# Kernel optimization log

Hardware: AMD Instinct MI355X
Metric: run time of the kernel (lower is better)

## Reference

```python
import jax, jax.numpy as jnp
import numpy as np

B, S, HID = 2, 1024, 2048
HQ, HKV, HD = 32, 8, 64
ROPE_BASE = 10000.0

def _rope_tables(seq_len, head_dim):
    inv_freq = 1.0 / (ROPE_BASE ** (np.arange(0, head_dim, 2, dtype=np.float32) / head_dim))
    t = np.arange(seq_len, dtype=np.float32)
    freqs = np.outer(t, inv_freq)                      # [S, d/2]
    emb = np.concatenate([freqs, freqs], axis=-1)      # [S, d]
    return jnp.asarray(np.cos(emb)), jnp.asarray(np.sin(emb))

def setup_inputs() -> dict:
    key = jax.random.key(0)
    ks = jax.random.split(key, 5)
    cos, sin = _rope_tables(S, HD)
    return {
        'hidden_states': jax.random.normal(ks[0], (B, S, HID), jnp.float32),
        'cos': cos, 'sin': sin,
        'Wq': jax.random.normal(ks[1], (HID, HID), jnp.float32) * (HID ** -0.5),
        'Wk': jax.random.normal(ks[2], (HID, HKV * HD), jnp.float32) * (HID ** -0.5),
        'Wv': jax.random.normal(ks[3], (HID, HKV * HD), jnp.float32) * (HID ** -0.5),
        'Wo': jax.random.normal(ks[4], (HID, HID), jnp.float32) * (HID ** -0.5),
    }

def _rotate_half(x):
    d = x.shape[-1]
    return jnp.concatenate([-x[..., d // 2:], x[..., :d // 2]], axis=-1)

def reference(hidden_states, cos, sin, Wq, Wk, Wv, Wo):
    b, s, _ = hidden_states.shape
    q = (hidden_states @ Wq).reshape(b, s, HQ, HD)    # [b,s,Hq,d]
    k = (hidden_states @ Wk).reshape(b, s, HKV, HD)   # [b,s,Hkv,d]
    v = (hidden_states @ Wv).reshape(b, s, HKV, HD)
    # RoPE: cos/sin [s,d] broadcast as [s,1,d] over head dim
    c = cos[:, None, :]
    sn = sin[:, None, :]
    q = q * c + _rotate_half(q) * sn
    k = k * c + _rotate_half(k) * sn
    # GQA: expand kv heads to query heads (repeat_kv)
    n_rep = HQ // HKV
    k = jnp.repeat(k, n_rep, axis=2)                  # [b,s,Hq,d]
    v = jnp.repeat(v, n_rep, axis=2)
    scale = HD ** -0.5
    scores = jnp.einsum('bqhd,bkhd->bhqk', q, k) * scale  # [b,Hq,s,s]
    causal = jnp.tril(jnp.ones((s, s), bool))
    scores = jnp.where(causal, scores, jnp.float32(-1e30))
    probs = jax.nn.softmax(scores.astype(jnp.float32), axis=-1).astype(q.dtype)
    out = jnp.einsum('bhqk,bkhd->bqhd', probs, v).reshape(b, s, HID)
    return out @ Wo
```

## Files before the change

kernel.cpp:

```cpp
#include <hip/hip_runtime.h>
#include <math.h>

#define B_   2
#define S_   1024
#define HID_ 2048
#define HQ_  32
#define HKV_ 8
#define HD_  64
#define NQKV 3072

using short8  = __attribute__((ext_vector_type(8))) short;
using floatx4 = __attribute__((ext_vector_type(4))) float;

__device__ __forceinline__ unsigned short f2bf(float x) {
    unsigned int u = __builtin_bit_cast(unsigned int, x);
    u += 0x7FFFu + ((u >> 16) & 1u);
    return (unsigned short)(u >> 16);
}
__device__ __forceinline__ float bf2f(unsigned short u) {
    return __builtin_bit_cast(float, (unsigned int)u << 16);
}

__device__ __forceinline__ void gl_lds16(const unsigned short* g, unsigned short* l) {
    __builtin_amdgcn_global_load_lds(
        (const __attribute__((address_space(1))) void*)g,
        (__attribute__((address_space(3))) void*)l, 16, 0, 0);
}

__global__ __launch_bounds__(256) void gemm_qkv(const unsigned short* __restrict__ A,
                                                const unsigned short* __restrict__ Bt,
                                                unsigned short* __restrict__ Qp,
                                                unsigned short* __restrict__ KVp) {
    __shared__ __align__(16) unsigned short As[128 * 32];
    __shared__ __align__(16) unsigned short Bs[128 * 32];

    int bid = blockIdx.x;
    int m0, n0, z, Nw, nc0;
    unsigned short* C;
    if (bid < 512) {
        n0 = (bid & 15) * 128; m0 = ((bid >> 4) & 15) * 128; z = bid >> 8;
        C = Qp + (size_t)z * 2048 * 2048; Nw = 2048; nc0 = n0;
    } else {
        bid -= 512;
        n0 = 2048 + (bid & 7) * 128; m0 = ((bid >> 3) & 15) * 128; z = bid >> 7;
        C = KVp + (size_t)z * 2048 * 1024; Nw = 1024; nc0 = n0 - 2048;
    }
    const int kbase = z * 1024;

    const int tid  = threadIdx.x;
    const int w    = tid >> 6;
    const int lane = tid & 63;
    const int col  = lane & 15;
    const int quad = lane >> 4;
    const int wm = (w >> 1) * 64;
    const int wn = (w & 1) * 64;

    const int srow = lane >> 2;
    const int skof = (lane & 3) * 8;
    const unsigned short* Ag = A  + (size_t)(m0 + srow) * HID_ + skof;
    const unsigned short* Bg = Bt + (size_t)(n0 + srow) * HID_ + skof;
    const int rb = w * 16;

    floatx4 acc[4][4] = {};

    for (int k0 = kbase; k0 < kbase + 1024; k0 += 32) {
        gl_lds16(Ag + (size_t)(rb     ) * HID_ + k0, &As[(rb     ) * 32]);
        gl_lds16(Ag + (size_t)(rb + 64) * HID_ + k0, &As[(rb + 64) * 32]);
        gl_lds16(Bg + (size_t)(rb     ) * HID_ + k0, &Bs[(rb     ) * 32]);
        gl_lds16(Bg + (size_t)(rb + 64) * HID_ + k0, &Bs[(rb + 64) * 32]);
        __syncthreads();

        short8 af[4], bfr[4];
#pragma unroll
        for (int i = 0; i < 4; ++i)
            af[i] = *(const short8*)&As[(wm + i * 16 + col) * 32 + quad * 8];
#pragma unroll
        for (int j = 0; j < 4; ++j)
            bfr[j] = *(const short8*)&Bs[(wn + j * 16 + col) * 32 + quad * 8];
#pragma unroll
        for (int i = 0; i < 4; ++i)
#pragma unroll
            for (int j = 0; j < 4; ++j)
                acc[i][j] = __builtin_amdgcn_mfma_f32_16x16x32_bf16(
                    af[i], bfr[j], acc[i][j], 0, 0, 0);
        __syncthreads();
    }

#pragma unroll
    for (int i = 0; i < 4; ++i)
#pragma unroll
        for (int j = 0; j < 4; ++j)
#pragma unroll
            for (int r = 0; r < 4; ++r)
                C[(size_t)(m0 + wm + i * 16 + quad * 4 + r) * Nw
                  + (nc0 + wn + j * 16 + col)] = f2bf(acc[i][j][r]);
}

__global__ __launch_bounds__(256) void gemm_wo(const unsigned short* __restrict__ A,
                                               const unsigned short* __restrict__ Bt,
                                               float* __restrict__ Cf,
                                               unsigned short* __restrict__ Cp1) {
    __shared__ __align__(16) unsigned short As[128 * 32];
    __shared__ __align__(16) unsigned short Bs[128 * 32];

    const int m0 = blockIdx.y * 128;
    const int n0 = blockIdx.x * 128;
    const int z  = blockIdx.z;
    const int kbase = z * 1024;

    const int tid  = threadIdx.x;
    const int w    = tid >> 6;
    const int lane = tid & 63;
    const int col  = lane & 15;
    const int quad = lane >> 4;
    const int wm = (w >> 1) * 64;
    const int wn = (w & 1) * 64;

    const int srow = lane >> 2;
    const int skof = (lane & 3) * 8;
    const unsigned short* Ag = A  + (size_t)(m0 + srow) * HID_ + skof;
    const unsigned short* Bg = Bt + (size_t)(n0 + srow) * HID_ + skof;
    const int rb = w * 16;

    floatx4 acc[4][4] = {};

    for (int k0 = kbase; k0 < kbase + 1024; k0 += 32) {
        gl_lds16(Ag + (size_t)(rb     ) * HID_ + k0, &As[(rb     ) * 32]);
        gl_lds16(Ag + (size_t)(rb + 64) * HID_ + k0, &As[(rb + 64) * 32]);
        gl_lds16(Bg + (size_t)(rb     ) * HID_ + k0, &Bs[(rb     ) * 32]);
        gl_lds16(Bg + (size_t)(rb + 64) * HID_ + k0, &Bs[(rb + 64) * 32]);
        __syncthreads();

        short8 af[4], bfr[4];
#pragma unroll
        for (int i = 0; i < 4; ++i)
            af[i] = *(const short8*)&As[(wm + i * 16 + col) * 32 + quad * 8];
#pragma unroll
        for (int j = 0; j < 4; ++j)
            bfr[j] = *(const short8*)&Bs[(wn + j * 16 + col) * 32 + quad * 8];
#pragma unroll
        for (int i = 0; i < 4; ++i)
#pragma unroll
            for (int j = 0; j < 4; ++j)
                acc[i][j] = __builtin_amdgcn_mfma_f32_16x16x32_bf16(
                    af[i], bfr[j], acc[i][j], 0, 0, 0);
        __syncthreads();
    }

#pragma unroll
    for (int i = 0; i < 4; ++i)
#pragma unroll
        for (int j = 0; j < 4; ++j)
#pragma unroll
            for (int r = 0; r < 4; ++r) {
                size_t off = (size_t)(m0 + wm + i * 16 + quad * 4 + r) * HID_
                           + (n0 + wn + j * 16 + col);
                if (z == 0) Cf[off] = acc[i][j][r];
                else        Cp1[off] = f2bf(acc[i][j][r]);
            }
}

__global__ __launch_bounds__(256) void reduce_wo(float* __restrict__ out,
                                                 const unsigned short* __restrict__ p1) {
    int i4 = (blockIdx.x * 256 + threadIdx.x) * 4;
    float4 o = *(float4*)&out[i4];
    ushort4 p = *(const ushort4*)&p1[i4];
    o.x += bf2f(p.x); o.y += bf2f(p.y); o.z += bf2f(p.z); o.w += bf2f(p.w);
    *(float4*)&out[i4] = o;
}

__global__ __launch_bounds__(256) void convert_x(const float* __restrict__ in,
                                                 unsigned short* __restrict__ out) {
    int tid = blockIdx.x * 256 + threadIdx.x;
    float4 v = *(const float4*)&in[(size_t)tid * 4];
    ushort4 o = {f2bf(v.x), f2bf(v.y), f2bf(v.z), f2bf(v.w)};
    *(ushort4*)&out[(size_t)tid * 4] = o;
}

__global__ __launch_bounds__(256) void transpose_qkv(const float* __restrict__ Wq,
                                                     const float* __restrict__ Wk,
                                                     const float* __restrict__ Wv,
                                                     unsigned short* __restrict__ WcatT) {
    __shared__ float tile[32][33];
    int bid = blockIdx.x;
    const float* W;
    unsigned short* WT;
    int N, tn0, tk0;
    if (bid < 4096) {
        W = Wq; WT = WcatT; N = HID_;
        tn0 = (bid & 63) * 32; tk0 = (bid >> 6) * 32;
    } else if (bid < 5120) {
        bid -= 4096;
        W = Wk; WT = WcatT + (size_t)HID_ * HID_; N = 512;
        tn0 = (bid & 15) * 32; tk0 = (bid >> 4) * 32;
    } else {
        bid -= 5120;
        W = Wv; WT = WcatT + (size_t)(HID_ + 512) * HID_; N = 512;
        tn0 = (bid & 15) * 32; tk0 = (bid >> 4) * 32;
    }
    const int r  = threadIdx.x >> 3;
    const int c4 = (threadIdx.x & 7) * 4;
    float4 v = *(const float4*)&W[(size_t)(tk0 + r) * N + tn0 + c4];
    tile[r][c4 + 0] = v.x;
    tile[r][c4 + 1] = v.y;
    tile[r][c4 + 2] = v.z;
    tile[r][c4 + 3] = v.w;
    __syncthreads();
    ushort4 o = {f2bf(tile[c4 + 0][r]), f2bf(tile[c4 + 1][r]),
                 f2bf(tile[c4 + 2][r]), f2bf(tile[c4 + 3][r])};
    *(ushort4*)&WT[(size_t)(tn0 + r) * HID_ + tk0 + c4] = o;
}

__global__ __launch_bounds__(256) void transpose_wo(const float* __restrict__ Wo,
                                                    unsigned short* __restrict__ WoT) {
    __shared__ float tile[32][33];
    int bid = blockIdx.x;
    const int tn0 = (bid & 63) * 32;
    const int tk0 = (bid >> 6) * 32;
    const int r  = threadIdx.x >> 3;
    const int c4 = (threadIdx.x & 7) * 4;
    float4 v = *(const float4*)&Wo[(size_t)(tk0 + r) * HID_ + tn0 + c4];
    tile[r][c4 + 0] = v.x;
    tile[r][c4 + 1] = v.y;
    tile[r][c4 + 2] = v.z;
    tile[r][c4 + 3] = v.w;
    __syncthreads();
    ushort4 o = {f2bf(tile[c4 + 0][r]), f2bf(tile[c4 + 1][r]),
                 f2bf(tile[c4 + 2][r]), f2bf(tile[c4 + 3][r])};
    *(ushort4*)&WoT[(size_t)(tn0 + r) * HID_ + tk0 + c4] = o;
}

__global__ __launch_bounds__(256) void convert_qkv(const unsigned short* __restrict__ Qp,
                                                   const unsigned short* __restrict__ KVp,
                                                   const float* __restrict__ cosT,
                                                   const float* __restrict__ sinT,
                                                   unsigned short* __restrict__ Qbf,
                                                   unsigned short* __restrict__ Kbf,
                                                   unsigned short* __restrict__ Vt) {
    const size_t QSTR  = (size_t)2048 * 2048;
    const size_t KVSTR = (size_t)2048 * 1024;
    int tid = blockIdx.x * 256 + threadIdx.x;
    const int NQ = B_ * S_ * HQ_ * 32;
    const int NK = B_ * S_ * HKV_ * 32;
    if (tid < NQ) {
        int d = tid & 31;
        int h = (tid >> 5) & (HQ_ - 1);
        int s = (tid >> 10) & (S_ - 1);
        int b = tid >> 20;
        const unsigned short* row = Qp + (size_t)(b * S_ + s) * 2048 + h * HD_;
        float x0 = bf2f(row[d])      + bf2f(row[QSTR + d]);
        float x1 = bf2f(row[d + 32]) + bf2f(row[QSTR + d + 32]);
        float c0 = cosT[s * HD_ + d],      s0 = sinT[s * HD_ + d];
        float c1 = cosT[s * HD_ + d + 32], s1 = sinT[s * HD_ + d + 32];
        unsigned short* orow = Qbf + ((size_t)(b * HQ_ + h) * S_ + s) * HD_;
        orow[d]      = f2bf((x0 * c0 - x1 * s0) * 0.125f);
        orow[d + 32] = f2bf((x1 * c1 + x0 * s1) * 0.125f);
    } else if (tid < NQ + NK) {
        tid -= NQ;
        int d  = tid & 31;
        int kv = (tid >> 5) & (HKV_ - 1);
        int s  = (tid >> 8) & (S_ - 1);
        int b  = tid >> 18;
        const unsigned short* row = KVp + (size_t)(b * S_ + s) * 1024 + kv * HD_;
        float x0 = bf2f(row[d])      + bf2f(row[KVSTR + d]);
        float x1 = bf2f(row[d + 32]) + bf2f(row[KVSTR + d + 32]);
        float c0 = cosT[s * HD_ + d],      s0 = sinT[s * HD_ + d];
        float c1 = cosT[s * HD_ + d + 32], s1 = sinT[s * HD_ + d + 32];
        unsigned short* orow = Kbf + ((size_t)(b * HKV_ + kv) * S_ + s) * HD_;
        orow[d]      = f2bf(x0 * c0 - x1 * s0);
        orow[d + 32] = f2bf(x1 * c1 + x0 * s1);
    } else {
        tid -= NQ + NK;
        int s4 = tid & 255;
        int d  = (tid >> 8) & (HD_ - 1);
        int kv = (tid >> 14) & (HKV_ - 1);
        int b  = tid >> 17;
        int s  = s4 * 4;
        const unsigned short* base =
            KVp + ((size_t)(b * S_ + s)) * 1024 + 512 + kv * HD_ + d;
        ushort4 o;
#pragma unroll
        for (int j = 0; j < 4; ++j) {
            float v = bf2f(base[(size_t)j * 1024]) +
                      bf2f(base[KVSTR + (size_t)j * 1024]);
            ((unsigned short*)&o)[j] = f2bf(v);
        }
        *(ushort4*)&Vt[((size_t)(b * HKV_ + kv) * HD_ + d) * S_ + s] = o;
    }
}

__global__ __launch_bounds__(256) void attn_mfma(const unsigned short* __restrict__ Qbf,
                                                 const unsigned short* __restrict__ Kbf,
                                                 const unsigned short* __restrict__ Vt,
                                                 unsigned short* __restrict__ Ctx) {
    const int t  = 63 - blockIdx.x;
    const int kv = blockIdx.y;
    const int b  = blockIdx.z;
    const int w    = threadIdx.x >> 6;
    const int lane = threadIdx.x & 63;
    const int col  = lane & 15;
    const int quad = lane >> 4;

    const int h   = kv * 4 + w;
    const int bh  = b * HQ_ + h;
    const int bkv = b * HKV_ + kv;
    const int qw  = 16 * t;
    const int myq = qw + col;

    __shared__ __align__(16) unsigned short sK[2][64 * 32];
    __shared__ __align__(16) unsigned short sV[2][64 * 32];
    __shared__ __align__(16) unsigned short sP[4][16 * 72];
    unsigned short* myP = sP[w];

    const unsigned short* qrow = Qbf + ((size_t)bh * S_ + qw + col) * HD_;
    short8 bq0 = *(const short8*)&qrow[quad * 8];
    short8 bq1 = *(const short8*)&qrow[32 + quad * 8];

    const unsigned short* Kbase = Kbf + (size_t)bkv * S_ * HD_;
    const unsigned short* Vbase = Vt  + (size_t)bkv * HD_ * S_;

    const int srow = 16 * w + (lane >> 2);
    const int sch  = (lane & 3) * 8;
    unsigned short* dK0 = &sK[0][16 * w * 32];
    unsigned short* dK1 = &sK[1][16 * w * 32];
    unsigned short* dV0 = &sV[0][16 * w * 32];
    unsigned short* dV1 = &sV[1][16 * w * 32];

    floatx4 acc[4] = {};
    float m_i = -1e30f, l_i = 0.f;
    const int nsteps = (16 * t + 79) >> 6;

    for (int it = 0; it < nsteps; ++it) {
        const int k0 = it * 64;
        gl_lds16(Kbase + (size_t)(k0 + srow) * HD_ + sch,      dK0);
        gl_lds16(Kbase + (size_t)(k0 + srow) * HD_ + 32 + sch, dK1);
        gl_lds16(Vbase + (size_t)srow * S_ + k0 + sch,         dV0);
        gl_lds16(Vbase + (size_t)srow * S_ + k0 + 32 + sch,    dV1);
        __syncthreads();

        floatx4 sc[4];
#pragma unroll
        for (int tt = 0; tt < 4; ++tt) {
            short8 ak0 = *(const short8*)&sK[0][(16 * tt + col) * 32 + quad * 8];
            short8 ak1 = *(const short8*)&sK[1][(16 * tt + col) * 32 + quad * 8];
            floatx4 z = {0.f, 0.f, 0.f, 0.f};
            z = __builtin_amdgcn_mfma_f32_16x16x32_bf16(ak0, bq0, z, 0, 0, 0);
            z = __builtin_amdgcn_mfma_f32_16x16x32_bf16(ak1, bq1, z, 0, 0, 0);
            sc[tt] = z;
        }
        if (k0 + 63 > qw) {
#pragma unroll
            for (int tt = 0; tt < 4; ++tt)
#pragma unroll
                for (int r = 0; r < 4; ++r)
                    if (k0 + 16 * tt + quad * 4 + r > myq) sc[tt][r] = -1e30f;
        }
        float vmax = sc[0][0];
#pragma unroll
        for (int tt = 0; tt < 4; ++tt)
#pragma unroll
            for (int r = 0; r < 4; ++r)
                vmax = fmaxf(vmax, sc[tt][r]);
        vmax = fmaxf(vmax, __shfl_xor(vmax, 16, 64));
        vmax = fmaxf(vmax, __shfl_xor(vmax, 32, 64));
        const float mnew  = fmaxf(m_i, vmax);
        const float alpha = __expf(m_i - mnew);
        m_i = mnew;
        float lsum = 0.f;
#pragma unroll
        for (int tt = 0; tt < 4; ++tt) {
            float p0 = __expf(sc[tt][0] - mnew);
            float p1 = __expf(sc[tt][1] - mnew);
            float p2 = __expf(sc[tt][2] - mnew);
            float p3 = __expf(sc[tt][3] - mnew);
            lsum += (p0 + p1) + (p2 + p3);
            ushort4 pk = {f2bf(p0), f2bf(p1), f2bf(p2), f2bf(p3)};
            *(ushort4*)&myP[col * 72 + 16 * tt + quad * 4] = pk;
        }
        lsum += __shfl_xor(lsum, 16, 64);
        lsum += __shfl_xor(lsum, 32, 64);
        l_i = l_i * alpha + lsum;
        float a_r[4];
#pragma unroll
        for (int r = 0; r < 4; ++r)
            a_r[r] = __shfl(alpha, quad * 4 + r, 64);
#pragma unroll
        for (int nt = 0; nt < 4; ++nt)
#pragma unroll
            for (int r = 0; r < 4; ++r)
                acc[nt][r] *= a_r[r];
        short8 pa0 = *(const short8*)&myP[col * 72 + quad * 8];
        short8 pa1 = *(const short8*)&myP[col * 72 + 32 + quad * 8];
#pragma unroll
        for (int nt = 0; nt < 4; ++nt) {
            short8 vb0 = *(const short8*)&sV[0][(nt * 16 + col) * 32 + quad * 8];
            short8 vb1 = *(const short8*)&sV[1][(nt * 16 + col) * 32 + quad * 8];
            acc[nt] = __builtin_amdgcn_mfma_f32_16x16x32_bf16(pa0, vb0, acc[nt], 0, 0, 0);
            acc[nt] = __builtin_amdgcn_mfma_f32_16x16x32_bf16(pa1, vb1, acc[nt], 0, 0, 0);
        }
        __syncthreads();
    }

    const float invl = 1.0f / l_i;
    float inv_r[4];
#pragma unroll
    for (int r = 0; r < 4; ++r)
        inv_r[r] = __shfl(invl, quad * 4 + r, 64);
#pragma unroll
    for (int nt = 0; nt < 4; ++nt)
#pragma unroll
        for (int r = 0; r < 4; ++r)
            Ctx[(size_t)(b * S_ + qw + quad * 4 + r) * HID_ + h * HD_ + nt * 16 + col] =
                f2bf(acc[nt][r] * inv_r[r]);
}

extern "C" void kernel_launch(void* const* d_in, const int* in_sizes, int n_in,
                              void* d_out, int out_size, void* d_ws, size_t ws_size,
                              hipStream_t stream) {
    const float* X    = (const float*)d_in[0];
    const float* cosT = (const float*)d_in[1];
    const float* sinT = (const float*)d_in[2];
    const float* Wq   = (const float*)d_in[3];
    const float* Wk   = (const float*)d_in[4];
    const float* Wv   = (const float*)d_in[5];
    const float* Wo   = (const float*)d_in[6];

    const int M = B_ * S_;
    const size_t MB = 1024u * 1024u;

    char* ws = (char*)d_ws;
    unsigned short* Xbf   = (unsigned short*)(ws);
    unsigned short* Qbf   = (unsigned short*)(ws);
    unsigned short* WcatT = (unsigned short*)(ws + 8 * MB);
    unsigned short* Kbf   = (unsigned short*)(ws + 8 * MB);
    unsigned short* Vt    = (unsigned short*)(ws + 10 * MB);
    unsigned short* WoT   = (unsigned short*)(ws + 12 * MB);
    unsigned short* KVp   = (unsigned short*)(ws + 20 * MB);
    unsigned short* Ctxbf = (unsigned short*)(ws + 20 * MB);
    unsigned short* Wop1  = (unsigned short*)(ws);
    unsigned short* Qp    = (unsigned short*)d_out;
    float* out = (float*)d_out;

    convert_x<<<(M * HID_ / 4) / 256, 256, 0, stream>>>(X, Xbf);

    transpose_qkv<<<6144, 256, 0, stream>>>(Wq, Wk, Wv, WcatT);

    gemm_qkv<<<768, 256, 0, stream>>>(Xbf, WcatT, Qp, KVp);

    {
        int total = B_ * S_ * HQ_ * 32 + B_ * S_ * HKV_ * 32
                  + B_ * HKV_ * HD_ * (S_ / 4);
        convert_qkv<<<total / 256, 256, 0, stream>>>(Qp, KVp, cosT, sinT,
                                                     Qbf, Kbf, Vt);
    }

    transpose_wo<<<4096, 256, 0, stream>>>(Wo, WoT);

    attn_mfma<<<dim3(64, HKV_, B_), 256, 0, stream>>>(Qbf, Kbf, Vt, Ctxbf);

    gemm_wo<<<dim3(16, 16, 2), 256, 0, stream>>>(Ctxbf, WoT, out, Wop1);

    reduce_wo<<<(M * HID_ / 4) / 256, 256, 0, stream>>>(out, Wop1);
}
```

Baseline: 246.9 us.

## Double-buffer K/V tiles, process two query tiles per wave, swizzle LDS

The attention kernel now gives each wave 32 query rows instead of 16, reusing every K/V LDS tile across two MFMA query tiles and halving the grid. K/V tiles are double-buffered, so the next tile's global-to-LDS load is issued before computing on the current one. LDS rows are widened to 64 elements with an XOR swizzle to avoid bank conflicts, and s_setprio raises priority around the MFMA sections. Costs are more registers and LDS per block and fewer blocks, which may lower occupancy and worsen load balance under the causal mask.

```diff
diff --git a/kernel.cpp b/kernel.cpp
--- a/kernel.cpp
+++ b/kernel.cpp
@@ -293,7 +293,7 @@
                                                  const unsigned short* __restrict__ Kbf,
                                                  const unsigned short* __restrict__ Vt,
                                                  unsigned short* __restrict__ Ctx) {
-    const int t  = 63 - blockIdx.x;
+    const int tq = 31 - blockIdx.x;
     const int kv = blockIdx.y;
     const int b  = blockIdx.z;
     const int w    = threadIdx.x >> 6;
@@ -304,114 +304,162 @@
     const int h   = kv * 4 + w;
     const int bh  = b * HQ_ + h;
     const int bkv = b * HKV_ + kv;
-    const int qw  = 16 * t;
-    const int myq = qw + col;
-
-    __shared__ __align__(16) unsigned short sK[2][64 * 32];
-    __shared__ __align__(16) unsigned short sV[2][64 * 32];
-    __shared__ __align__(16) unsigned short sP[4][16 * 72];
+    const int qw  = 32 * tq;
+
+    __shared__ __align__(16) unsigned short sK[2][64 * 64];
+    __shared__ __align__(16) unsigned short sV[2][64 * 64];
+    __shared__ __align__(16) unsigned short sP[4][32 * 72];
     unsigned short* myP = sP[w];
 
-    const unsigned short* qrow = Qbf + ((size_t)bh * S_ + qw + col) * HD_;
-    short8 bq0 = *(const short8*)&qrow[quad * 8];
-    short8 bq1 = *(const short8*)&qrow[32 + quad * 8];
+    short8 bq[2][2];
+#pragma unroll
+    for (int u = 0; u < 2; ++u) {
+        const unsigned short* qrow = Qbf + ((size_t)bh * S_ + qw + 16 * u + col) * HD_;
+        bq[u][0] = *(const short8*)&qrow[quad * 8];
+        bq[u][1] = *(const short8*)&qrow[32 + quad * 8];
+    }
 
     const unsigned short* Kbase = Kbf + (size_t)bkv * S_ * HD_;
     const unsigned short* Vbase = Vt  + (size_t)bkv * HD_ * S_;
 
-    const int srow = 16 * w + (lane >> 2);
-    const int sch  = (lane & 3) * 8;
-    unsigned short* dK0 = &sK[0][16 * w * 32];
-    unsigned short* dK1 = &sK[1][16 * w * 32];
-    unsigned short* dV0 = &sV[0][16 * w * 32];
-    unsigned short* dV1 = &sV[1][16 * w * 32];
-
-    floatx4 acc[4] = {};
-    float m_i = -1e30f, l_i = 0.f;
-    const int nsteps = (16 * t + 79) >> 6;
-
+    const int sr  = lane >> 3;
+    const int ssl = (lane & 7) ^ sr;
+    const int r0  = 16 * w;
+
+    floatx4 acc[2][4] = {};
+    float m_i[2] = {-1e30f, -1e30f};
+    float l_i[2] = {0.f, 0.f};
+
+    const int nsteps = (qw + 95) >> 6;
+
+#pragma unroll
+    for (int c = 0; c < 2; ++c) {
+        const int row = r0 + 8 * c + sr;
+        gl_lds16(Kbase + (size_t)row * HD_ + ssl * 8, &sK[0][(r0 + 8 * c) * 64]);
+        gl_lds16(Vbase + (size_t)row * S_ + ssl * 8,  &sV[0][(r0 + 8 * c) * 64]);
+    }
+    __syncthreads();
+
+    int cur = 0;
     for (int it = 0; it < nsteps; ++it) {
         const int k0 = it * 64;
-        gl_lds16(Kbase + (size_t)(k0 + srow) * HD_ + sch,      dK0);
-        gl_lds16(Kbase + (size_t)(k0 + srow) * HD_ + 32 + sch, dK1);
-        gl_lds16(Vbase + (size_t)srow * S_ + k0 + sch,         dV0);
-        gl_lds16(Vbase + (size_t)srow * S_ + k0 + 32 + sch,    dV1);
+
+        if (it + 1 < nsteps) {
+            const int kn = k0 + 64;
+#pragma unroll
+            for (int c = 0; c < 2; ++c) {
+                const int row = r0 + 8 * c + sr;
+                gl_lds16(Kbase + (size_t)(kn + row) * HD_ + ssl * 8,
+                         &sK[cur ^ 1][(r0 + 8 * c) * 64]);
+                gl_lds16(Vbase + (size_t)row * S_ + kn + ssl * 8,
+                         &sV[cur ^ 1][(r0 + 8 * c) * 64]);
+            }
+        }
+
+        floatx4 sc[2][4];
+        __builtin_amdgcn_s_setprio(1);
+#pragma unroll
+        for (int tt = 0; tt < 4; ++tt) {
+            const int krow = 16 * tt + col;
+            const unsigned short* kr = &sK[cur][krow * 64];
+            short8 ak0 = *(const short8*)&kr[((quad    ) ^ (krow & 7)) * 8];
+            short8 ak1 = *(const short8*)&kr[((quad + 4) ^ (krow & 7)) * 8];
+#pragma unroll
+            for (int u = 0; u < 2; ++u) {
+                floatx4 z = {0.f, 0.f, 0.f, 0.f};
+                z = __builtin_amdgcn_mfma_f32_16x16x32_bf16(ak0, bq[u][0], z, 0, 0, 0);
+                z = __builtin_amdgcn_mfma_f32_16x16x32_bf16(ak1, bq[u][1], z, 0, 0, 0);
+                sc[u][tt] = z;
+            }
+        }
+        __builtin_amdgcn_s_setprio(0);
+
+#pragma unroll
+        for (int u = 0; u < 2; ++u) {
+            const int qbase = qw + 16 * u;
+            const int myq   = qbase + col;
+            if (k0 + 63 > qbase) {
+#pragma unroll
+                for (int tt = 0; tt < 4; ++tt)
+#pragma unroll
+                    for (int r = 0; r < 4; ++r)
+                        if (k0 + 16 * tt + quad * 4 + r > myq) sc[u][tt][r] = -1e30f;
+            }
+            float vmax = sc[u][0][0];
+#pragma unroll
+            for (int tt = 0; tt < 4; ++tt)
+#pragma unroll
+                for (int r = 0; r < 4; ++r)
+                    vmax = fmaxf(vmax, sc[u][tt][r]);
+            vmax = fmaxf(vmax, __shfl_xor(vmax, 16, 64));
+            vmax = fmaxf(vmax, __shfl_xor(vmax, 32, 64));
+            const float mnew  = fmaxf(m_i[u], vmax);
+            const float alpha = __expf(m_i[u] - mnew);
+            m_i[u] = mnew;
+            float lsum = 0.f;
+#pragma unroll
+            for (int tt = 0; tt < 4; ++tt) {
+                float p0 = __expf(sc[u][tt][0] - mnew);
+                float p1 = __expf(sc[u][tt][1] - mnew);
+                float p2 = __expf(sc[u][tt][2] - mnew);
+                float p3 = __expf(sc[u][tt][3] - mnew);
+                lsum += (p0 + p1) + (p2 + p3);
+                ushort4 pk = {f2bf(p0), f2bf(p1), f2bf(p2), f2bf(p3)};
+                *(ushort4*)&myP[(16 * u + col) * 72 + 16 * tt + quad * 4] = pk;
+            }
+            lsum += __shfl_xor(lsum, 16, 64);
+            lsum += __shfl_xor(lsum, 32, 64);
+            l_i[u] = l_i[u] * alpha + lsum;
+            float a_r[4];
+#pragma unroll
+            for (int r = 0; r < 4; ++r)
+                a_r[r] = __shfl(alpha, quad * 4 + r, 64);
+#pragma unroll
+            for (int nt = 0; nt < 4; ++nt)
+#pragma unroll
+                for (int r = 0; r < 4; ++r)
+                    acc[u][nt][r] *= a_r[r];
+        }
+
+        short8 pa[2][2];
+#pragma unroll
+        for (int u = 0; u < 2; ++u) {
+            pa[u][0] = *(const short8*)&myP[(16 * u + col) * 72 + quad * 8];
+            pa[u][1] = *(const short8*)&myP[(16 * u + col) * 72 + 32 + quad * 8];
+        }
+        __builtin_amdgcn_s_setprio(1);
+#pragma unroll
+        for (int nt = 0; nt < 4; ++nt) {
+            const int vrow = 16 * nt + col;
+            const unsigned short* vr = &sV[cur][vrow * 64];
+            short8 vb0 = *(const short8*)&vr[((quad    ) ^ (vrow & 7)) * 8];
+            short8 vb1 = *(const short8*)&vr[((quad + 4) ^ (vrow & 7)) * 8];
+#pragma unroll
+            for (int u = 0; u < 2; ++u) {
+                acc[u][nt] = __builtin_amdgcn_mfma_f32_16x16x32_bf16(pa[u][0], vb0, acc[u][nt], 0, 0, 0);
+                acc[u][nt] = __builtin_amdgcn_mfma_f32_16x16x32_bf16(pa[u][1], vb1, acc[u][nt], 0, 0, 0);
+            }
+        }
+        __builtin_amdgcn_s_setprio(0);
+
         __syncthreads();
-
-        floatx4 sc[4];
-#pragma unroll
-        for (int tt = 0; tt < 4; ++tt) {
-            short8 ak0 = *(const short8*)&sK[0][(16 * tt + col) * 32 + quad * 8];
-            short8 ak1 = *(const short8*)&sK[1][(16 * tt + col) * 32 + quad * 8];
-            floatx4 z = {0.f, 0.f, 0.f, 0.f};
-            z = __builtin_amdgcn_mfma_f32_16x16x32_bf16(ak0, bq0, z, 0, 0, 0);
-            z = __builtin_amdgcn_mfma_f32_16x16x32_bf16(ak1, bq1, z, 0, 0, 0);
-            sc[tt] = z;
-        }
-        if (k0 + 63 > qw) {
-#pragma unroll
-            for (int tt = 0; tt < 4; ++tt)
-#pragma unroll
-                for (int r = 0; r < 4; ++r)
-                    if (k0 + 16 * tt + quad * 4 + r > myq) sc[tt][r] = -1e30f;
-        }
-        float vmax = sc[0][0];
-#pragma unroll
-        for (int tt = 0; tt < 4; ++tt)
+        cur ^= 1;
+    }
+
+#pragma unroll
+    for (int u = 0; u < 2; ++u) {
+        const float invl = 1.0f / l_i[u];
+        float inv_r[4];
+#pragma unroll
+        for (int r = 0; r < 4; ++r)
+            inv_r[r] = __shfl(invl, quad * 4 + r, 64);
+#pragma unroll
+        for (int nt = 0; nt < 4; ++nt)
 #pragma unroll
             for (int r = 0; r < 4; ++r)
-                vmax = fmaxf(vmax, sc[tt][r]);
-        vmax = fmaxf(vmax, __shfl_xor(vmax, 16, 64));
-        vmax = fmaxf(vmax, __shfl_xor(vmax, 32, 64));
-        const float mnew  = fmaxf(m_i, vmax);
-        const float alpha = __expf(m_i - mnew);
-        m_i = mnew;
-        float lsum = 0.f;
-#pragma unroll
-        for (int tt = 0; tt < 4; ++tt) {
-            float p0 = __expf(sc[tt][0] - mnew);
-            float p1 = __expf(sc[tt][1] - mnew);
-            float p2 = __expf(sc[tt][2] - mnew);
-            float p3 = __expf(sc[tt][3] - mnew);
-            lsum += (p0 + p1) + (p2 + p3);
-            ushort4 pk = {f2bf(p0), f2bf(p1), f2bf(p2), f2bf(p3)};
-            *(ushort4*)&myP[col * 72 + 16 * tt + quad * 4] = pk;
-        }
-        lsum += __shfl_xor(lsum, 16, 64);
-        lsum += __shfl_xor(lsum, 32, 64);
-        l_i = l_i * alpha + lsum;
-        float a_r[4];
-#pragma unroll
-        for (int r = 0; r < 4; ++r)
-            a_r[r] = __shfl(alpha, quad * 4 + r, 64);
-#pragma unroll
-        for (int nt = 0; nt < 4; ++nt)
-#pragma unroll
-            for (int r = 0; r < 4; ++r)
-                acc[nt][r] *= a_r[r];
-        short8 pa0 = *(const short8*)&myP[col * 72 + quad * 8];
-        short8 pa1 = *(const short8*)&myP[col * 72 + 32 + quad * 8];
-#pragma unroll
-        for (int nt = 0; nt < 4; ++nt) {
-            short8 vb0 = *(const short8*)&sV[0][(nt * 16 + col) * 32 + quad * 8];
-            short8 vb1 = *(const short8*)&sV[1][(nt * 16 + col) * 32 + quad * 8];
-            acc[nt] = __builtin_amdgcn_mfma_f32_16x16x32_bf16(pa0, vb0, acc[nt], 0, 0, 0);
-            acc[nt] = __builtin_amdgcn_mfma_f32_16x16x32_bf16(pa1, vb1, acc[nt], 0, 0, 0);
-        }
-        __syncthreads();
-    }
-
-    const float invl = 1.0f / l_i;
-    float inv_r[4];
-#pragma unroll
-    for (int r = 0; r < 4; ++r)
-        inv_r[r] = __shfl(invl, quad * 4 + r, 64);
-#pragma unroll
-    for (int nt = 0; nt < 4; ++nt)
-#pragma unroll
-        for (int r = 0; r < 4; ++r)
-            Ctx[(size_t)(b * S_ + qw + quad * 4 + r) * HID_ + h * HD_ + nt * 16 + col] =
-                f2bf(acc[nt][r] * inv_r[r]);
+                Ctx[(size_t)(b * S_ + qw + 16 * u + quad * 4 + r) * HID_
+                    + h * HD_ + nt * 16 + col] = f2bf(acc[u][nt][r] * inv_r[r]);
+    }
 }
 
 extern "C" void kernel_launch(void* const* d_in, const int* in_sizes, int n_in,
@@ -456,7 +504,7 @@
 
     transpose_wo<<<4096, 256, 0, stream>>>(Wo, WoT);
 
-    attn_mfma<<<dim3(64, HKV_, B_), 256, 0, stream>>>(Qbf, Kbf, Vt, Ctxbf);
+    attn_mfma<<<dim3(32, HKV_, B_), 256, 0, stream>>>(Qbf, Kbf, Vt, Ctxbf);
 
     gemm_wo<<<dim3(16, 16, 2), 256, 0, stream>>>(Ctxbf, WoT, out, Wop1);
 
```

Measured after the change: 245.8 us. No clear change (-0.4%).
